# Optimization experiments

Measured on AMD Instinct MI355X. Metric: run time of the kernel, lower is better.

## Reference

```python
import jax, jax.numpy as jnp
import numpy as np

# Model hyperparameters (match init_kwargs)
H, DK, DV, L = 16, 64, 64, 512   # num_heads, dim_key, dim_value, segment_len
B, S, D = 4, 8192, 1024          # batch, seq_len, dim_input (H*DK == D)


def setup_inputs() -> dict:
    key = jax.random.key(0)
    k = jax.random.split(key, 6)
    w = 0.02  # init scale for projection weights
    return {
        "x": jax.random.normal(k[0], (B, S, D), jnp.float32),
        "Wq": jax.random.normal(k[1], (D, H * DK), jnp.float32) * w,
        "Wk": jax.random.normal(k[2], (D, H * DK), jnp.float32) * w,
        "Wv": jax.random.normal(k[3], (D, H * DV), jnp.float32) * w,
        "Wo": jax.random.normal(k[4], (H * DV, D), jnp.float32) * w,
        "betas": jax.random.normal(k[5], (1, H, 1, DV), jnp.float32),
    }


def reference(x, Wq, Wk, Wv, Wo, betas):
    Bx, Sx, Dx = x.shape
    n_seg = Sx // L
    xs = x.reshape(Bx, n_seg, L, Dx)

    def proj(W, dh):
        p = jnp.einsum('bnld,df->bnlf', xs, W)                 # [B,n,L,H*dh]
        # torch does .view(B, H, L, dh) on [B, L, H*dh] -- a raw row-major
        # reshape (NOT the usual head split), replicated faithfully here.
        return p.reshape(Bx, n_seg, H, L, dh).transpose(1, 0, 2, 3, 4)  # [n,B,H,L,dh]

    q = proj(Wq, DK)
    k = proj(Wk, DK)
    v = proj(Wv, DV)
    gate = jax.nn.sigmoid(betas)                               # [1,H,1,DV]
    scale = 1.0 / jnp.sqrt(jnp.float32(DK))

    def step(carry, qkv):
        mem, zc = carry                                        # mem [B,H,DK,DV], zc [B,H,1,DK]
        qs, ks, vs = qkv                                       # each [B,H,L,d]
        sq = jax.nn.elu(qs) + 1.0
        # 'linear' memory update
        mem = mem + jnp.einsum('bhsk,bhsv->bhkv', sq, vs)
        zc = zc + (jax.nn.elu(ks) + 1.0).sum(axis=-2, keepdims=True)
        # local softmax attention
        scores = jnp.einsum('bhsk,bhtk->bhst', qs, ks) * scale
        att_dot = jnp.einsum('bhst,bhtv->bhsv', jax.nn.softmax(scores, axis=-1), vs)
        # memory retrieval; in torch z is [B,H,DV,DK] with identical rows (zc
        # broadcast), so sigma_q @ z == sigma_q.sum(-1) * zc (needs DK == DV).
        num = jnp.einsum('bhsk,bhkv->bhsv', sq, mem)
        den = sq.sum(axis=-1, keepdims=True) * zc              # [B,H,L,DK]
        att = gate * (num / den) + (1.0 - gate) * att_dot      # [B,H,L,DV]
        out_seg = att.reshape(Bx, L, H * DV) @ Wo              # raw reshape, as torch .view
        return (mem, zc), out_seg

    mem0 = jnp.zeros((Bx, H, DK, DV), x.dtype)
    zc0 = jnp.zeros((Bx, H, 1, DK), x.dtype)
    _, outs = jax.lax.scan(step, (mem0, zc0), (q, k, v))       # outs [n,B,L,D]
    return outs.transpose(1, 0, 2, 3).reshape(Bx, Sx, Dx)
```

## Files before the change

kernel.cpp:

```cpp
#include <hip/hip_runtime.h>
#include <hip/hip_bf16.h>

typedef unsigned short u16;
typedef unsigned int u32;
typedef short bf16x8 __attribute__((ext_vector_type(8)));
typedef float floatx4 __attribute__((ext_vector_type(4)));

#define BB 4
#define SS 8192
#define DD 1024
#define HH 16
#define DKV 64
#define LL 512
#define NSEG 16
#define MROWS 32768

__device__ __forceinline__ float bf2f(u16 u){
  union { u32 i; float f; } v; v.i = ((u32)u) << 16; return v.f;
}
__device__ __forceinline__ u16 f2bf(float f){
  union { float f; u32 i; } v; v.f = f;
  u32 r = v.i + 0x7FFF + ((v.i >> 16) & 1);
  return (u16)(r >> 16);
}

__device__ __forceinline__ void store_out(u16* p, float v){ *p = f2bf(v); }
__device__ __forceinline__ void store_out(float* p, float v){ *p = v; }

__device__ __forceinline__ void gload_lds16(const u16* g, u16* l){
  __builtin_amdgcn_global_load_lds(
      (const __attribute__((address_space(1))) void*)g,
      (__attribute__((address_space(3))) void*)l, 16, 0, 0);
}

__global__ __launch_bounds__(256) void cvt_f32_bf16(const float* __restrict__ X,
                                                    u16* __restrict__ Xb){
  const int tid = blockIdx.x * 256 + threadIdx.x;
#pragma unroll
  for (int it = 0; it < 8; it++){
    size_t base = (size_t)it * 4194304 + (size_t)tid * 8;
    float4 f0 = *(const float4*)(X + base);
    float4 f1 = *(const float4*)(X + base + 4);
    bf16x8 o;
    o[0] = (short)f2bf(f0.x); o[1] = (short)f2bf(f0.y);
    o[2] = (short)f2bf(f0.z); o[3] = (short)f2bf(f0.w);
    o[4] = (short)f2bf(f1.x); o[5] = (short)f2bf(f1.y);
    o[6] = (short)f2bf(f1.z); o[7] = (short)f2bf(f1.w);
    *(bf16x8*)(Xb + base) = o;
  }
}

__global__ __launch_bounds__(256) void transpose_w(const float* __restrict__ W,
                                                   u16* __restrict__ WT){
  __shared__ __align__(16) u16 tile[64*65];
  const int bid = blockIdx.x;
  const int br = (bid >> 4) * 64, bc = (bid & 15) * 64;
  const int t = threadIdx.x;
#pragma unroll
  for (int i = 0; i < 16; i++){
    int idx = i*256 + t; int r = idx >> 6, c = idx & 63;
    tile[r*65 + c] = f2bf(W[(size_t)(br + r)*1024 + bc + c]);
  }
  __syncthreads();
#pragma unroll
  for (int i = 0; i < 16; i++){
    int idx = i*256 + t; int r = idx >> 6, c = idx & 63;
    WT[(size_t)(bc + r)*1024 + br + c] = tile[c*65 + r];
  }
}

template <typename OT>
__global__ __launch_bounds__(256) void gemm_bt(const u16* __restrict__ A,
                                               const u16* __restrict__ Bt,
                                               OT* __restrict__ C,
                                               int Mdim, int Ndim, int Kdim){
  __shared__ __align__(16) u16 As[128*32];
  __shared__ __align__(16) u16 Bs[128*32];
  const int nt = Ndim >> 7;
  const int bm = blockIdx.x / nt, bn = blockIdx.x % nt;
  const int t = threadIdx.x, lane = t & 63, w = t >> 6;
  const int low = lane & 15, quad = lane >> 4;
  const int wm = w >> 1, wn = w & 1;
  const size_t m0 = (size_t)bm * 128, n0 = (size_t)bn * 128;
  const int rA = lane >> 2;
  const int cA = (lane & 3) * 8;

  floatx4 acc[4][4];
#pragma unroll
  for (int i = 0; i < 4; i++)
#pragma unroll
    for (int j = 0; j < 4; j++) acc[i][j] = (floatx4)(0.0f);

  for (int kt = 0; kt < Kdim; kt += 32){
    const int cc0 = w*2, cc1 = w*2 + 1;
    gload_lds16(A  + (m0 + cc0*16 + rA)*Kdim + kt + cA, &As[cc0*512]);
    gload_lds16(A  + (m0 + cc1*16 + rA)*Kdim + kt + cA, &As[cc1*512]);
    gload_lds16(Bt + (n0 + cc0*16 + rA)*Kdim + kt + cA, &Bs[cc0*512]);
    gload_lds16(Bt + (n0 + cc1*16 + rA)*Kdim + kt + cA, &Bs[cc1*512]);
    __syncthreads();
    bf16x8 af[4], bfr[4];
#pragma unroll
    for (int mi = 0; mi < 4; mi++)
      af[mi] = *(const bf16x8*)&As[(wm*64 + mi*16 + low)*32 + quad*8];
#pragma unroll
    for (int ni = 0; ni < 4; ni++)
      bfr[ni] = *(const bf16x8*)&Bs[(wn*64 + ni*16 + low)*32 + quad*8];
#pragma unroll
    for (int mi = 0; mi < 4; mi++)
#pragma unroll
      for (int ni = 0; ni < 4; ni++)
        acc[mi][ni] = __builtin_amdgcn_mfma_f32_16x16x32_bf16(af[mi], bfr[ni], acc[mi][ni], 0, 0, 0);
    __syncthreads();
  }
#pragma unroll
  for (int mi = 0; mi < 4; mi++){
    size_t row = m0 + wm*64 + mi*16 + quad*4;
#pragma unroll
    for (int ni = 0; ni < 4; ni++){
      size_t col = n0 + wn*64 + ni*16 + low;
#pragma unroll
      for (int r = 0; r < 4; r++)
        store_out(&C[(row + r)*(size_t)Ndim + col], acc[mi][ni][r]);
    }
  }
}

__global__ __launch_bounds__(256) void seg_mem(const u16* __restrict__ Pq,
                                               const u16* __restrict__ Pk,
                                               const u16* __restrict__ Pv,
                                               float* __restrict__ Mc,
                                               float* __restrict__ Zs){
  __shared__ float sqb[64*65];
  __shared__ float vsb[64*65];
  __shared__ float red[256];
  const int bid = blockIdx.x;
  const int n = bid & 15, h = (bid >> 4) & 15, b = bid >> 8;
  const size_t chunk = ((size_t)((b*16 + n)*16 + h)) * 32768;
  const u16* qc = Pq + chunk;
  const u16* kc = Pk + chunk;
  const u16* vc = Pv + chunk;
  const int t = threadIdx.x;
  const int tv = t >> 4, tk = t & 15;
  float acc[4][4];
#pragma unroll
  for (int i = 0; i < 4; i++)
#pragma unroll
    for (int j = 0; j < 4; j++) acc[i][j] = 0.f;
  float zacc = 0.f;

  for (int c = 0; c < 8; c++){
    __syncthreads();
#pragma unroll
    for (int i = 0; i < 16; i++){
      int idx = i*256 + t;
      int l = idx >> 6, k = idx & 63;
      float x = bf2f(qc[c*4096 + idx]);
      sqb[l*65 + k] = x > 0.f ? x + 1.f : __expf(x);
      vsb[l*65 + k] = bf2f(vc[c*4096 + idx]);
      float kx = bf2f(kc[c*4096 + idx]);
      zacc += kx > 0.f ? kx + 1.f : __expf(kx);
    }
    __syncthreads();
#pragma unroll 4
    for (int l = 0; l < 64; l++){
      float vv[4], sv[4];
#pragma unroll
      for (int i = 0; i < 4; i++) vv[i] = vsb[l*65 + tv*4 + i];
#pragma unroll
      for (int j = 0; j < 4; j++) sv[j] = sqb[l*65 + tk*4 + j];
#pragma unroll
      for (int i = 0; i < 4; i++)
#pragma unroll
        for (int j = 0; j < 4; j++) acc[i][j] += vv[i]*sv[j];
    }
  }
  float* mco = Mc + (size_t)(((b*16 + h)*16 + n)) * 4096;
#pragma unroll
  for (int i = 0; i < 4; i++)
#pragma unroll
    for (int j = 0; j < 4; j++)
      mco[(tv*4 + i)*64 + tk*4 + j] = acc[i][j];

  red[t] = zacc;
  __syncthreads();
  if (t < 64)
    Zs[(size_t)(((b*16 + h)*16 + n))*64 + t] = red[t] + red[t+64] + red[t+128] + red[t+192];
}

__global__ __launch_bounds__(256) void prefix_mem(const float* __restrict__ Mc,
                                                  const float* __restrict__ Zs,
                                                  u16* __restrict__ MemT,
                                                  float* __restrict__ Zc){
  const int bh = blockIdx.x >> 2, sub = blockIdx.x & 3;
  const int t = threadIdx.x;
#pragma unroll
  for (int i = 0; i < 4; i++){
    int e = (sub*4 + i)*256 + t;
    float run = 0.f;
    for (int n = 0; n < 16; n++){
      size_t off = ((size_t)(bh*16 + n))*4096 + e;
      run += Mc[off];
      MemT[off] = f2bf(run);
    }
  }
  if (sub == 0 && t < 64){
    float run = 0.f;
    for (int n = 0; n < 16; n++){
      size_t off = ((size_t)(bh*16 + n))*64 + t;
      run += Zs[off];
      Zc[off] = run;
    }
  }
}

#define CPAD 136
__global__ __launch_bounds__(256, 3) void attn_seg(const u16* __restrict__ Pq,
                                                   const u16* __restrict__ Pk,
                                                   const u16* __restrict__ Pv,
                                                   const u16* __restrict__ MemT,
                                                   const float* __restrict__ Zc,
                                                   const float* __restrict__ betas,
                                                   u16* __restrict__ Att){
  __shared__ __align__(16) u16 vsTc[64 * CPAD];
  __shared__ __align__(16) u16 Pbuf[4 * 16 * CPAD];
  __shared__ float ws_sq[64];

  const int t = threadIdx.x, lane = t & 63, w = t >> 6;
  const int low = lane & 15, quad = lane >> 4;
  const int p = blockIdx.x;
  const int cidx = (p & 7) * 128 + (p >> 6);
  const int st   = (p >> 3) & 7;
  const int h = cidx & 15, n = (cidx >> 4) & 15, b = cidx >> 8;

  const size_t chunk = ((size_t)((b*16 + n)*16 + h)) * 32768;
  const u16* qc = Pq + chunk;
  const u16* kc = Pk + chunk;
  const u16* vc = Pv + chunk;
  u16* ac = Att + chunk;
  const int mzidx = (b*16 + h)*16 + n;
  const u16* memt = MemT + (size_t)mzidx * 4096;
  const float* zc = Zc + (size_t)mzidx * 64;
  const int srow0 = st*64 + w*16;

  bf16x8 qf[2], sqf[2];
  float sqsum = 0.f;
#pragma unroll
  for (int kk = 0; kk < 2; kk++){
    qf[kk] = *(const bf16x8*)(qc + (srow0 + low)*64 + kk*32 + quad*8);
    bf16x8 sf;
#pragma unroll
    for (int j = 0; j < 8; j++){
      float x = bf2f((u16)qf[kk][j]);
      float s = x > 0.f ? x + 1.f : __expf(x);
      sqsum += s;
      sf[j] = (short)f2bf(s);
    }
    sqf[kk] = sf;
  }
  sqsum += __shfl_xor(sqsum, 16);
  sqsum += __shfl_xor(sqsum, 32);
  if (quad == 0) ws_sq[w*16 + low] = sqsum;

  u16* pb = &Pbuf[w * 16 * CPAD];
  floatx4 accd[4];
#pragma unroll
  for (int vt = 0; vt < 4; vt++) accd[vt] = (floatx4)(0.0f);
  float sm[4] = {0.f, 0.f, 0.f, 0.f};

  for (int c = 0; c < 4; c++){
#pragma unroll
    for (int i = 0; i < 16; i++){
      int idx = i*256 + t;
      int v = idx & 63;
      int lp = idx >> 6;
      int l = c*128 + 2*lp;
      u32 lo = vc[l*64 + v];
      u32 hi = vc[(l + 1)*64 + v];
      *(u32*)&vsTc[v*CPAD + 2*lp] = lo | (hi << 16);
    }
    floatx4 sc[8];
#pragma unroll
    for (int jc = 0; jc < 8; jc++){
      int j = c*8 + jc;
      bf16x8 b0 = *(const bf16x8*)(kc + (j*16 + low)*64 + quad*8);
      bf16x8 b1 = *(const bf16x8*)(kc + (j*16 + low)*64 + 32 + quad*8);
      floatx4 z = (floatx4)(0.0f);
      z = __builtin_amdgcn_mfma_f32_16x16x32_bf16(qf[0], b0, z, 0, 0, 0);
      sc[jc] = __builtin_amdgcn_mfma_f32_16x16x32_bf16(qf[1], b1, z, 0, 0, 0);
    }
#pragma unroll
    for (int jc = 0; jc < 8; jc++)
#pragma unroll
      for (int r = 0; r < 4; r++){
        float e = __expf(sc[jc][r] * 0.125f);
        sm[r] += e;
        pb[(quad*4 + r)*CPAD + jc*16 + low] = f2bf(e);
      }
    __syncthreads();
#pragma unroll
    for (int jj = 0; jj < 4; jj++){
      bf16x8 af = *(const bf16x8*)&pb[low*CPAD + jj*32 + quad*8];
#pragma unroll
      for (int vt = 0; vt < 4; vt++){
        bf16x8 bv = *(const bf16x8*)&vsTc[(vt*16 + low)*CPAD + jj*32 + quad*8];
        accd[vt] = __builtin_amdgcn_mfma_f32_16x16x32_bf16(af, bv, accd[vt], 0, 0, 0);
      }
    }
    __syncthreads();
  }

#pragma unroll
  for (int m = 1; m < 16; m <<= 1)
#pragma unroll
    for (int r = 0; r < 4; r++) sm[r] += __shfl_xor(sm[r], m);
  float inv[4];
#pragma unroll
  for (int r = 0; r < 4; r++) inv[r] = 1.f / sm[r];
#pragma unroll
  for (int vt = 0; vt < 4; vt++)
#pragma unroll
    for (int r = 0; r < 4; r++) accd[vt][r] *= inv[r];

  floatx4 accn[4];
#pragma unroll
  for (int vt = 0; vt < 4; vt++) accn[vt] = (floatx4)(0.0f);
#pragma unroll
  for (int kk = 0; kk < 2; kk++)
#pragma unroll
    for (int vt = 0; vt < 4; vt++){
      bf16x8 bm = *(const bf16x8*)(memt + (vt*16 + low)*64 + kk*32 + quad*8);
      accn[vt] = __builtin_amdgcn_mfma_f32_16x16x32_bf16(sqf[kk], bm, accn[vt], 0, 0, 0);
    }

#pragma unroll
  for (int vt = 0; vt < 4; vt++){
    int v = vt*16 + low;
    float zcv = zc[v];
    float beta = betas[h*64 + v];
    float g = 1.f / (1.f + __expf(-beta));
#pragma unroll
    for (int r = 0; r < 4; r++){
      float sqs = ws_sq[w*16 + quad*4 + r];
      float den = sqs * zcv;
      float att = g * (accn[vt][r] / den) + (1.f - g) * accd[vt][r];
      ac[(size_t)(srow0 + quad*4 + r)*64 + v] = f2bf(att);
    }
  }
}

extern "C" void kernel_launch(void* const* d_in, const int* in_sizes, int n_in,
                              void* d_out, int out_size, void* d_ws, size_t ws_size,
                              hipStream_t stream){
  const float* x     = (const float*)d_in[0];
  const float* Wq    = (const float*)d_in[1];
  const float* Wk    = (const float*)d_in[2];
  const float* Wv    = (const float*)d_in[3];
  const float* Wo    = (const float*)d_in[4];
  const float* betas = (const float*)d_in[5];

  unsigned char* w8 = (unsigned char*)d_ws;
  u16*   Xb   = (u16*)(w8 + 0);
  float* Mc   = (float*)(w8 + 0);
  u16*   MemT = (u16*)(w8 + (16ull << 20));
  float* Zs   = (float*)(w8 + (24ull << 20));
  float* Zc   = (float*)(w8 + (24ull << 20) + (256ull << 10));
  u16*   WqT  = (u16*)(w8 + (64ull << 20));
  u16*   WkT  = (u16*)(w8 + (66ull << 20));
  u16*   WvT  = (u16*)(w8 + (68ull << 20));
  u16*   WoT  = (u16*)(w8 + (70ull << 20));
  u16*   Pq   = (u16*)(w8 + (72ull  << 20));
  u16*   Pk   = (u16*)(w8 + (136ull << 20));
  u16*   Pv   = (u16*)(w8 + (200ull << 20));
  u16*   AttB = Pq;

  hipLaunchKernelGGL(cvt_f32_bf16, dim3(2048), dim3(256), 0, stream, x, Xb);

  hipLaunchKernelGGL(transpose_w, dim3(256), dim3(256), 0, stream, Wq, WqT);
  hipLaunchKernelGGL(transpose_w, dim3(256), dim3(256), 0, stream, Wk, WkT);
  hipLaunchKernelGGL(transpose_w, dim3(256), dim3(256), 0, stream, Wv, WvT);
  hipLaunchKernelGGL(transpose_w, dim3(256), dim3(256), 0, stream, Wo, WoT);

  hipLaunchKernelGGL(gemm_bt<u16>, dim3(2048), dim3(256), 0, stream, Xb, WqT, Pq, MROWS, DD, DD);
  hipLaunchKernelGGL(gemm_bt<u16>, dim3(2048), dim3(256), 0, stream, Xb, WkT, Pk, MROWS, DD, DD);
  hipLaunchKernelGGL(gemm_bt<u16>, dim3(2048), dim3(256), 0, stream, Xb, WvT, Pv, MROWS, DD, DD);

  hipLaunchKernelGGL(seg_mem, dim3(1024), dim3(256), 0, stream, Pq, Pk, Pv, Mc, Zs);
  hipLaunchKernelGGL(prefix_mem, dim3(256), dim3(256), 0, stream, Mc, Zs, MemT, Zc);
  hipLaunchKernelGGL(attn_seg, dim3(8192), dim3(256), 0, stream, Pq, Pk, Pv, MemT, Zc, betas, AttB);

  hipLaunchKernelGGL(gemm_bt<float>, dim3(2048), dim3(256), 0, stream, AttB, WoT, (float*)d_out, MROWS, DD, DD);
}
```

Before: 1.171 ms.

## Swizzle attention LDS tiles, prefetch V with vector loads, raise occupancy

Replaces the padded LDS layouts for the transposed V tile and the probability buffer with XOR-swizzled unpadded layouts. V is now fetched with 16-byte vector loads into registers and prefetched one chunk ahead, replacing the scalar 2-byte gather-and-pack loop. The row sums of sq move from shared memory to lane shuffles, the score exp is fused into the MFMA loop, MFMA priority is raised around the PV product, and launch bounds go from 3 to 4 blocks per CU. This targets global-load inefficiency and LDS bank conflicts, at the cost of more registers for the prefetch and possible spills under the tighter occupancy bound.

Measured after the change: 1.258 ms. 7.4% more time.

```diff
diff --git a/kernel.cpp b/kernel.cpp
--- a/kernel.cpp
+++ b/kernel.cpp
@@ -213,20 +213,19 @@
   }
 }
 
-#define CPAD 136
-__global__ __launch_bounds__(256, 3) void attn_seg(const u16* __restrict__ Pq,
+__global__ __launch_bounds__(256, 4) void attn_seg(const u16* __restrict__ Pq,
                                                    const u16* __restrict__ Pk,
                                                    const u16* __restrict__ Pv,
                                                    const u16* __restrict__ MemT,
                                                    const float* __restrict__ Zc,
                                                    const float* __restrict__ betas,
                                                    u16* __restrict__ Att){
-  __shared__ __align__(16) u16 vsTc[64 * CPAD];
-  __shared__ __align__(16) u16 Pbuf[4 * 16 * CPAD];
-  __shared__ float ws_sq[64];
+  __shared__ __align__(16) u16 vsTc[64 * 128];
+  __shared__ __align__(16) u16 Pbuf[4 * 16 * 128];
 
   const int t = threadIdx.x, lane = t & 63, w = t >> 6;
   const int low = lane & 15, quad = lane >> 4;
+  const int lo3 = low >> 3, lo7 = low & 7;
   const int p = blockIdx.x;
   const int cidx = (p & 7) * 128 + (p >> 6);
   const int st   = (p >> 3) & 7;
@@ -242,6 +241,10 @@
   const float* zc = Zc + (size_t)mzidx * 64;
   const int srow0 = st*64 + w*16;
 
+  const int skb = lane & 7;
+  const int sl7 = lane >> 3;
+  const int sv0 = skb * 8;
+
   bf16x8 qf[2], sqf[2];
   float sqsum = 0.f;
 #pragma unroll
@@ -259,9 +262,16 @@
   }
   sqsum += __shfl_xor(sqsum, 16);
   sqsum += __shfl_xor(sqsum, 32);
-  if (quad == 0) ws_sq[w*16 + low] = sqsum;
-
-  u16* pb = &Pbuf[w * 16 * CPAD];
+  float sqs[4];
+#pragma unroll
+  for (int r = 0; r < 4; r++) sqs[r] = __shfl(sqsum, quad*4 + r);
+
+  bf16x8 vld[4];
+#pragma unroll
+  for (int i = 0; i < 4; i++)
+    vld[i] = *(const bf16x8*)(vc + (i*32 + w*8 + sl7)*64 + sv0);
+
+  u16* pb = &Pbuf[w * 16 * 128];
   floatx4 accd[4];
 #pragma unroll
   for (int vt = 0; vt < 4; vt++) accd[vt] = (floatx4)(0.0f);
@@ -269,43 +279,48 @@
 
   for (int c = 0; c < 4; c++){
 #pragma unroll
-    for (int i = 0; i < 16; i++){
-      int idx = i*256 + t;
-      int v = idx & 63;
-      int lp = idx >> 6;
-      int l = c*128 + 2*lp;
-      u32 lo = vc[l*64 + v];
-      u32 hi = vc[(l + 1)*64 + v];
-      *(u32*)&vsTc[v*CPAD + 2*lp] = lo | (hi << 16);
-    }
-    floatx4 sc[8];
+    for (int i = 0; i < 4; i++){
+      const int u = i*4 + w;
+#pragma unroll
+      for (int j = 0; j < 8; j++){
+        vsTc[(sv0 + j)*128 + ((u ^ j ^ skb) << 3) + sl7] = (u16)vld[i][j];
+      }
+    }
+    if (c < 3){
+#pragma unroll
+      for (int i = 0; i < 4; i++)
+        vld[i] = *(const bf16x8*)(vc + ((c+1)*128 + i*32 + w*8 + sl7)*64 + sv0);
+    }
 #pragma unroll
     for (int jc = 0; jc < 8; jc++){
-      int j = c*8 + jc;
-      bf16x8 b0 = *(const bf16x8*)(kc + (j*16 + low)*64 + quad*8);
-      bf16x8 b1 = *(const bf16x8*)(kc + (j*16 + low)*64 + 32 + quad*8);
+      const int jg = c*8 + jc;
+      bf16x8 b0 = *(const bf16x8*)(kc + (jg*16 + low)*64 + quad*8);
+      bf16x8 b1 = *(const bf16x8*)(kc + (jg*16 + low)*64 + 32 + quad*8);
       floatx4 z = (floatx4)(0.0f);
       z = __builtin_amdgcn_mfma_f32_16x16x32_bf16(qf[0], b0, z, 0, 0, 0);
-      sc[jc] = __builtin_amdgcn_mfma_f32_16x16x32_bf16(qf[1], b1, z, 0, 0, 0);
-    }
-#pragma unroll
-    for (int jc = 0; jc < 8; jc++)
+      z = __builtin_amdgcn_mfma_f32_16x16x32_bf16(qf[1], b1, z, 0, 0, 0);
+      const int pcol = (((jc*2 + lo3) ^ (quad*2)) << 3) + lo7;
 #pragma unroll
       for (int r = 0; r < 4; r++){
-        float e = __expf(sc[jc][r] * 0.125f);
+        float e = __expf(z[r] * 0.125f);
         sm[r] += e;
-        pb[(quad*4 + r)*CPAD + jc*16 + low] = f2bf(e);
+        pb[(quad*4 + r)*128 + pcol] = f2bf(e);
       }
-    __syncthreads();
+    }
+    __syncthreads();
+    __builtin_amdgcn_s_setprio(1);
 #pragma unroll
     for (int jj = 0; jj < 4; jj++){
-      bf16x8 af = *(const bf16x8*)&pb[low*CPAD + jj*32 + quad*8];
+      const int unit = jj*4 + quad;
+      bf16x8 af = *(const bf16x8*)&pb[low*128 + ((unit ^ ((low >> 2) << 1)) << 3)];
 #pragma unroll
       for (int vt = 0; vt < 4; vt++){
-        bf16x8 bv = *(const bf16x8*)&vsTc[(vt*16 + low)*CPAD + jj*32 + quad*8];
+        const int kv = lo7 ^ (vt*2 + lo3);
+        bf16x8 bv = *(const bf16x8*)&vsTc[(vt*16 + low)*128 + ((unit ^ kv) << 3)];
         accd[vt] = __builtin_amdgcn_mfma_f32_16x16x32_bf16(af, bv, accd[vt], 0, 0, 0);
       }
     }
+    __builtin_amdgcn_s_setprio(0);
     __syncthreads();
   }
 
@@ -340,8 +355,7 @@
     float g = 1.f / (1.f + __expf(-beta));
 #pragma unroll
     for (int r = 0; r < 4; r++){
-      float sqs = ws_sq[w*16 + quad*4 + r];
-      float den = sqs * zcv;
+      float den = sqs[r] * zcv;
       float att = g * (accn[vt][r] / den) + (1.f - g) * accd[vt][r];
       ac[(size_t)(srow0 + quad*4 + r)*64 + v] = f2bf(att);
     }
```
